# Kernel tuning notes

Hardware: AMD Instinct MI355X
Metric: run time of the kernel (lower is better)

The kernel has to match this reference:

```python
import jax, jax.numpy as jnp
import numpy as np

TWO_PI = 2.0 * np.pi
ALPHA = 0.65
KSIZE = (3, 3, 3)   # (kOr, kH, kW)
ITERS = 1
BN_EPS = 1e-5


def _interp(v, dy, dx):
    """Bilinear sample of v[b,c,o, y+dy[o], x+dx[o]], border-clamped.
    v: [B,C,Or,H,W]; dy, dx: [Or] float per-orientation constant shifts."""
    H, W = v.shape[3], v.shape[4]
    y0 = jnp.floor(dy); fy = dy - y0; y0 = y0.astype(jnp.int32)
    iy = jnp.arange(H)[None, :] + y0[:, None]                      # [Or,H]
    g0 = jnp.take_along_axis(v, jnp.clip(iy, 0, H - 1)[None, None, :, :, None], axis=3)
    g1 = jnp.take_along_axis(v, jnp.clip(iy + 1, 0, H - 1)[None, None, :, :, None], axis=3)
    fyb = fy[None, None, :, None, None]
    v = (1.0 - fyb) * g0 + fyb * g1
    x0 = jnp.floor(dx); fx = dx - x0; x0 = x0.astype(jnp.int32)
    ix = jnp.arange(W)[None, :] + x0[:, None]                      # [Or,W]
    h0 = jnp.take_along_axis(v, jnp.clip(ix, 0, W - 1)[None, None, :, None, :], axis=4)
    h1 = jnp.take_along_axis(v, jnp.clip(ix + 1, 0, W - 1)[None, None, :, None, :], axis=4)
    fxb = fx[None, None, :, None, None]
    return (1.0 - fxb) * h0 + fxb * h1


def _convection(u, g0):
    """out[b,c,p] = u[b,c, p . g0[c]^{-1}] via trilinear resampling.
    Sample point: ((x,y) - R(theta - th0)@(x0,y0), theta - th0), theta periodic."""
    Or = u.shape[2]
    def one(uc, g):  # uc: [B,Or,H,W], g = (x0, y0, th0)
        x0, y0, th0 = g[0], g[1], g[2]
        t = th0 * Or / TWO_PI
        i = jnp.floor(t); f = t - i; i = i.astype(jnp.int32)
        # periodic linear interpolation along orientation axis
        v = (1.0 - f) * jnp.roll(uc, i, axis=1) + f * jnp.roll(uc, i + 1, axis=1)
        a = jnp.arange(Or, dtype=u.dtype) * (TWO_PI / Or) - th0
        dx = -(jnp.cos(a) * x0 - jnp.sin(a) * y0)
        dy = -(jnp.sin(a) * x0 + jnp.cos(a) * y0)
        return _interp(v[:, None], dy, dx)[:, 0]
    return jax.vmap(one, in_axes=(1, 0), out_axes=1)(u, g0)


def _se2_log(qx, qy, dth):
    """Exact SE(2) logarithm coordinates (c1,c2,c3) of group offset (qx,qy,dth)."""
    if abs(dth) < 1e-9:
        return qx, qy, dth
    h = 0.5 * dth
    cot = np.cos(h) / np.sin(h)
    return h * (qx * cot + qy), h * (-qx + qy * cot), dth


def _morph(u, metric, dilate):
    """Fractional morphological dilation (max of u(p.q) - k(q)) or erosion
    (min of u(p.q) + k(q)) with left-invariant Riemannian kernel
    k_c(q) = nu_a * d_c(q)^{2a/(2a-1)}, d_c^2 = (m0*c1)^2+(m1*c2)^2+(m2*c3)^2."""
    kOr, kH, kW = KSIZE
    Or = u.shape[2]
    thetas = jnp.arange(Or, dtype=u.dtype) * (TWO_PI / Or)
    p = 2.0 * ALPHA / (2.0 * ALPHA - 1.0)
    nu = (2.0 * ALPHA - 1.0) * (2.0 * ALPHA) ** (-p)
    out = None
    for qt in range(-(kOr // 2), kOr // 2 + 1):
        dth = qt * TWO_PI / Or
        for qy in range(-(kH // 2), kH // 2 + 1):
            for qx in range(-(kW // 2), kW // 2 + 1):
                c1, c2, c3 = _se2_log(float(qx), float(qy), dth)
                s = (metric[:, 0] * c1) ** 2 + (metric[:, 1] * c2) ** 2 + (metric[:, 2] * c3) ** 2
                k = nu * s ** (p / 2.0)                       # [C]
                # left-invariant shift: spatial offset rotated by theta_o
                dxo = jnp.cos(thetas) * qx - jnp.sin(thetas) * qy
                dyo = jnp.sin(thetas) * qx + jnp.cos(thetas) * qy
                val = _interp(jnp.roll(u, -qt, axis=2), dyo, dxo)
                kb = k[None, :, None, None, None]
                cand = val - kb if dilate else val + kb
                if out is None:
                    out = cand
                else:
                    out = jnp.maximum(out, cand) if dilate else jnp.minimum(out, cand)
    return out


def setup_inputs() -> dict:
    key = jax.random.key(0)
    ks = jax.random.split(key, 5)
    B, Cin, Cout, Or, H, W = 4, 8, 16, 8, 128, 128
    x = jax.random.normal(ks[0], (B, Cin, Or, H, W), dtype=jnp.float32)
    g0 = 0.5 * jax.random.normal(ks[1], (Cin, 3), dtype=jnp.float32)
    lo, hi = 1.4 / 3.0, 0.7 * 3.0   # reset_parameters range for metric params
    metric_dil = jax.random.uniform(ks[2], (Cin, 3), minval=lo, maxval=hi, dtype=jnp.float32)
    metric_ero = jax.random.uniform(ks[3], (Cin, 3), minval=lo, maxval=hi, dtype=jnp.float32)
    bound = 0.25  # kaiming_uniform(a=sqrt(5)) bound for [8,16] weight
    weight = jax.random.uniform(ks[4], (Cin, Cout), minval=-bound, maxval=bound, dtype=jnp.float32)
    gamma = jnp.ones((Cout,), jnp.float32)
    beta = jnp.zeros((Cout,), jnp.float32)
    return dict(x=x, g0=g0, metric_dil=metric_dil, metric_ero=metric_ero,
                weight=weight, gamma=gamma, beta=beta)


def reference(x, g0, metric_dil, metric_ero, weight, gamma, beta):
    u = x
    for _ in range(ITERS):
        u = _convection(u, g0)
        u = _morph(u, metric_dil, dilate=True)
        u = _morph(u, metric_ero, dilate=False)
    # channel mixing: [B,Cin,Or,H,W] x [Cin,Cout] -> [B,Cout,Or,H,W]
    y = jnp.einsum('bcohw,cd->bdohw', u, weight)
    # BatchNorm3d (training mode): per-channel stats over (B,Or,H,W)
    m = y.mean(axis=(0, 2, 3, 4), keepdims=True)
    v = y.var(axis=(0, 2, 3, 4), keepdims=True)
    yh = (y - m) * jax.lax.rsqrt(v + BN_EPS)
    return yh * gamma[None, :, None, None, None] + beta[None, :, None, None, None]
```

## Files before the change

### kernel.cpp

```cpp
#include <hip/hip_runtime.h>
#include <math.h>
#include <utility>

#define B 4
#define CIN 8
#define COUT 16
#define OR_ 8
#define H_ 128
#define W_ 128
#define HW 16384
#define PLANE HW
#define CH_STR (OR_*HW)
#define BATCH_STR (CIN*CH_STR)
#define NELEM (B*BATCH_STR)
#define NPOS (B*OR_*HW)
#define NB_RED 256

#define TILE 16
#define CBR 24
#define CB_S 29
#define CB_PL (CBR*CB_S)
#define DBR 20
#define DB_S 21
#define DB_PL (DBR*DB_S)

typedef __attribute__((ext_vector_type(4))) float f4;

struct Tables {
  float kdil[CIN][27];
  float kero[CIN][27];
  int   o1[CIN][OR_], o2[CIN][OR_];
  int   iy0[CIN][OR_], ix0[CIN][OR_];
  float w00[CIN][OR_], w01[CIN][OR_], w10[CIN][OR_], w11[CIN][OR_];
  float cf[CIN];
};

__host__ __device__ constexpr double m_cos(int o) {
  const double r = 0.70710678118654752440;
  const double t[8] = {1.0, r, 0.0, -r, -1.0, -r, 0.0, r};
  return t[o];
}
__host__ __device__ constexpr double m_sin(int o) {
  const double r = 0.70710678118654752440;
  const double t[8] = {0.0, r, 1.0, r, 0.0, -r, -1.0, -r};
  return t[o];
}
__host__ __device__ constexpr double tap_dx(int o, int j) {
  return m_cos(o)*(j % 3 - 1) - m_sin(o)*(j / 3 - 1);
}
__host__ __device__ constexpr double tap_dy(int o, int j) {
  return m_sin(o)*(j % 3 - 1) + m_cos(o)*(j / 3 - 1);
}
__host__ __device__ constexpr int ifloor(double v) {
  int i = (int)v;
  return ((double)i > v) ? i - 1 : i;
}
__host__ __device__ constexpr int tap_ix(int o, int j) { return ifloor(tap_dx(o, j)); }
__host__ __device__ constexpr int tap_iy(int o, int j) { return ifloor(tap_dy(o, j)); }
__host__ __device__ constexpr float tap_fx(int o, int j) { return (float)(tap_dx(o, j) - tap_ix(o, j)); }
__host__ __device__ constexpr float tap_fy(int o, int j) { return (float)(tap_dy(o, j) - tap_iy(o, j)); }
__host__ __device__ constexpr float corner_w(int o, int j, int dyb, int dxb) {
  float fy = tap_fy(o, j), fx = tap_fx(o, j);
  return (dyb ? fy : 1.0f - fy) * (dxb ? fx : 1.0f - fx);
}
__host__ __device__ constexpr int corner_r(int o, int j, int dyb) { return tap_iy(o, j) + dyb + 2; }
__host__ __device__ constexpr int corner_c(int o, int j, int i, int dxb) { return i + tap_ix(o, j) + dxb + 2; }
__host__ __device__ constexpr bool row_used(int o, int r) {
  for (int j = 0; j < 9; ++j)
    for (int dyb = 0; dyb < 2; ++dyb)
      for (int dxb = 0; dxb < 2; ++dxb)
        if (corner_w(o, j, dyb, dxb) != 0.0f && corner_r(o, j, dyb) == r)
          return true;
  return false;
}

template<int N> struct Rep {
  template<class F> __device__ __forceinline__ static void run(F&& f) {
    Rep<N-1>::run(f);
    f(std::integral_constant<int, N-1>{});
  }
};
template<> struct Rep<0> {
  template<class F> __device__ __forceinline__ static void run(F&&) {}
};


__global__ void precompute_kernel(const float* __restrict__ g0,
                                  const float* __restrict__ mdil,
                                  const float* __restrict__ mero,
                                  Tables* __restrict__ T) {
  const int t = threadIdx.x;
  const double TWO_PI = 6.283185307179586476925286766559;
  const double P  = 2.0*0.65/(2.0*0.65 - 1.0);
  const double NU = (2.0*0.65 - 1.0)*pow(2.0*0.65, -P);
  if (t < 432) {
    int which = t / 216;
    int r = t % 216;
    int c = r / 27;
    int j = r % 27;
    int qt = j/9 - 1;
    int qy = (j/3)%3 - 1;
    int qx = j%3 - 1;
    double dth = qt * (TWO_PI/OR_);
    double c1, c2, c3;
    if (qt == 0) { c1 = qx; c2 = qy; c3 = 0.0; }
    else {
      double h = 0.5*dth;
      double cot = cos(h)/sin(h);
      c1 = h*(qx*cot + qy);
      c2 = h*(-qx + qy*cot);
      c3 = dth;
    }
    const float* m = which ? mero : mdil;
    double a0 = (double)m[c*3+0]*c1;
    double a1 = (double)m[c*3+1]*c2;
    double a2 = (double)m[c*3+2]*c3;
    double s = a0*a0 + a1*a1 + a2*a2;
    float k = (float)(NU * pow(s, P*0.5));
    if (which) T->kero[c][j] = k; else T->kdil[c][j] = k;
  } else if (t >= 512 && t < 512 + CIN*OR_) {
    int r = t - 512;
    int c = r >> 3;
    int o = r & 7;
    float x0 = g0[c*3+0], y0 = g0[c*3+1], th0 = g0[c*3+2];
    float a = (float)(o*(TWO_PI/OR_)) - th0;
    float ca = cosf(a), sa = sinf(a);
    float dxv = -(ca*x0 - sa*y0);
    float dyv = -(sa*x0 + ca*y0);
    float fy0 = floorf(dyv), fx0 = floorf(dxv);
    float fy = dyv - fy0, fx = dxv - fx0;
    T->iy0[c][o] = (int)fy0;
    T->ix0[c][o] = (int)fx0;
    T->w00[c][o] = (1.f-fy)*(1.f-fx);
    T->w01[c][o] = (1.f-fy)*fx;
    T->w10[c][o] = fy*(1.f-fx);
    T->w11[c][o] = fy*fx;
    float tt = th0 * (float)(OR_/TWO_PI);
    float fi = floorf(tt);
    int ci = (int)fi;
    T->o1[c][o] = (o - ci) & 7;
    T->o2[c][o] = (o - ci - 1) & 7;
    if (o == 0) T->cf[c] = tt - fi;
  }
}

template<int O, int DIL, int PL, int RSTR>
__device__ __forceinline__ void morph_tile_lds(const float* __restrict__ sm,
                                               const float* __restrict__ kt,
                                               int row, int gc, float acc[4]) {
  Rep<3>::run([&](auto qc) {
    constexpr int qti = decltype(qc)::value;
    const float* p = sm + ((O + qti + 7) & 7) * PL + row * RSTR + gc;
    float win[5][8];
    Rep<5>::run([&](auto rc) {
      constexpr int r = decltype(rc)::value;
      if constexpr (row_used(O, r)) {
        #pragma unroll
        for (int k = 0; k < 8; ++k) win[r][k] = p[r*RSTR + k];
      }
    });
    Rep<9>::run([&](auto jc) {
      constexpr int j = decltype(jc)::value;
      float k = kt[qti*9 + j];
      float base = DIL ? -k : k;
      Rep<4>::run([&](auto ic) {
        constexpr int i = decltype(ic)::value;
        float v = base;
        Rep<4>::run([&](auto cc2) {
          constexpr int dyb = decltype(cc2)::value >> 1, dxb = decltype(cc2)::value & 1;
          constexpr float Wgt = corner_w(O, j, dyb, dxb);
          if constexpr (Wgt != 0.0f) {
            constexpr int R = corner_r(O, j, dyb);
            constexpr int C = corner_c(O, j, i, dxb);
            v = fmaf(Wgt, win[R][C], v);
          }
        });
        acc[i] = DIL ? fmaxf(acc[i], v) : fminf(acc[i], v);
      });
    });
  });
}

template<int O>
__device__ __forceinline__ void dil_wave(const float* __restrict__ cb, float* __restrict__ db,
                                         const float* __restrict__ kt, int lane) {
  {
    int rA = lane / 5, cA = (lane - rA*5) * 4;
    float acc[4] = {-INFINITY, -INFINITY, -INFINITY, -INFINITY};
    morph_tile_lds<O, 1, CB_PL, CB_S>(cb, kt, rA, cA, acc);
    float* d = db + O*DB_PL + rA*DB_S + cA;
    #pragma unroll
    for (int i = 0; i < 4; ++i) d[i] = acc[i];
  }
  if (lane < 36) {
    int g = lane + 64;
    int rB = g / 5, cB = (g - rB*5) * 4;
    float acc[4] = {-INFINITY, -INFINITY, -INFINITY, -INFINITY};
    morph_tile_lds<O, 1, CB_PL, CB_S>(cb, kt, rB, cB, acc);
    float* d = db + O*DB_PL + rB*DB_S + cB;
    #pragma unroll
    for (int i = 0; i < 4; ++i) d[i] = acc[i];
  }
}

template<int O>
__device__ __forceinline__ void ero_wave(const float* __restrict__ db, float* __restrict__ dst,
                                         const float* __restrict__ kt, int lane) {
  int pr = lane >> 2, pc = (lane & 3) * 4;
  float acc[4] = {INFINITY, INFINITY, INFINITY, INFINITY};
  morph_tile_lds<O, 0, DB_PL, DB_S>(db, kt, pr, pc, acc);
  f4 v = {acc[0], acc[1], acc[2], acc[3]};
  *(f4*)(dst + pr*W_ + pc) = v;
}

__global__ __launch_bounds__(512, 4)
void fused_kernel(const float* __restrict__ x, float* __restrict__ u3,
                  const Tables* __restrict__ T) {
  __shared__ float convbuf[8*CB_PL];
  __shared__ float dilbuf[8*DB_PL];

  int blk = blockIdx.x;
  int tx = blk & 7, ty = (blk >> 3) & 7, c = (blk >> 6) & 7, b = blk >> 9;
  int h0 = ty*TILE, w0 = tx*TILE;
  int t = threadIdx.x;
  int wid = t >> 6, lane = t & 63;

  {
    const int o = wid;
    const float* p1 = x + b*BATCH_STR + c*CH_STR + T->o1[c][o]*PLANE;
    const float* p2 = x + b*BATCH_STR + c*CH_STR + T->o2[c][o]*PLANE;
    const int iy0 = T->iy0[c][o], ix0 = T->ix0[c][o];
    const float w00 = T->w00[c][o], w01 = T->w01[c][o];
    const float w10 = T->w10[c][o], w11 = T->w11[c][o];
    const float cfv = T->cf[c];
    float* cbf = convbuf + o*CB_PL;
    #pragma unroll
    for (int it = 0; it < 3; ++it) {
      int q = lane + it*64;
      if (q < 144) {
        int r = q / 6, cq = q - r*6;
        int gr = h0 - 4 + r;
        int gc4 = w0 - 4 + cq*4;
        int iy = gr + iy0, ix = gc4 + ix0;
        bool ok = (gr >= 0) & (gr <= 127) & (gc4 >= 0) & (gc4+3 <= 127)
                & (iy >= 0) & (iy <= 126) & (ix >= 0) & (ix+4 <= 127);
        float* dst = cbf + r*CB_S + cq*4;
        if (ok) {
          const float* q1 = p1 + iy*W_ + ix;
          const float* q2 = p2 + iy*W_ + ix;
          f4 A0 = *(const f4*)q1;       float A4 = q1[4];
          f4 B0 = *(const f4*)(q1+W_);  float B4 = q1[W_+4];
          f4 C0 = *(const f4*)q2;       float C4 = q2[4];
          f4 D0 = *(const f4*)(q2+W_);  float D4 = q2[W_+4];
          float a[5] = {A0.x, A0.y, A0.z, A0.w, A4};
          float bb[5] = {B0.x, B0.y, B0.z, B0.w, B4};
          float cc[5] = {C0.x, C0.y, C0.z, C0.w, C4};
          float dd[5] = {D0.x, D0.y, D0.z, D0.w, D4};
          #pragma unroll
          for (int i = 0; i < 4; ++i) {
            float v1 = w00*a[i] + w01*a[i+1] + w10*bb[i] + w11*bb[i+1];
            float v2 = w00*cc[i] + w01*cc[i+1] + w10*dd[i] + w11*dd[i+1];
            dst[i] = (1.0f - cfv)*v1 + cfv*v2;
          }
        } else {
          int gh = min(max(gr, 0), 127);
          #pragma unroll
          for (int i = 0; i < 4; ++i) {
            int gw = min(max(gc4 + i, 0), 127);
            int yy = gh + iy0, xx = gw + ix0;
            int r0 = min(max(yy, 0), 127), r1 = min(max(yy+1, 0), 127);
            int c0 = min(max(xx, 0), 127), c1 = min(max(xx+1, 0), 127);
            float v1 = w00*p1[r0*W_+c0] + w01*p1[r0*W_+c1] + w10*p1[r1*W_+c0] + w11*p1[r1*W_+c1];
            float v2 = w00*p2[r0*W_+c0] + w01*p2[r0*W_+c1] + w10*p2[r1*W_+c0] + w11*p2[r1*W_+c1];
            dst[i] = (1.0f - cfv)*v1 + cfv*v2;
          }
        }
      }
    }
  }
  __syncthreads();

  {
    const float* kt = T->kdil[c];
    switch (wid) {
      case 0: dil_wave<0>(convbuf, dilbuf, kt, lane); break;
      case 1: dil_wave<1>(convbuf, dilbuf, kt, lane); break;
      case 2: dil_wave<2>(convbuf, dilbuf, kt, lane); break;
      case 3: dil_wave<3>(convbuf, dilbuf, kt, lane); break;
      case 4: dil_wave<4>(convbuf, dilbuf, kt, lane); break;
      case 5: dil_wave<5>(convbuf, dilbuf, kt, lane); break;
      case 6: dil_wave<6>(convbuf, dilbuf, kt, lane); break;
      default: dil_wave<7>(convbuf, dilbuf, kt, lane); break;
    }
  }
  __syncthreads();

  if ((h0 == 0) | (h0 == 112) | (w0 == 0) | (w0 == 112)) {
    #pragma unroll
    for (int k2 = 0; k2 < 7; ++k2) {
      int i = t + k2*512;
      if (i < 3200) {
        int o = i / 400, rest = i - o*400;
        int row = rest / 20, col = rest - row*20;
        int vh = h0 - 2 + row, vw = w0 - 2 + col;
        int dr = min(max(vh, 0), 127) - vh;
        int dc = min(max(vw, 0), 127) - vw;
        if ((dr | dc) != 0) {
          dilbuf[o*DB_PL + row*DB_S + col] =
            dilbuf[o*DB_PL + (row + dr)*DB_S + col + dc];
        }
      }
    }
  }
  __syncthreads();

  {
    const float* kt = T->kero[c];
    float* dst = u3 + ((b*CIN + c)*OR_ + wid)*PLANE + h0*W_ + w0;
    switch (wid) {
      case 0: ero_wave<0>(dilbuf, dst, kt, lane); break;
      case 1: ero_wave<1>(dilbuf, dst, kt, lane); break;
      case 2: ero_wave<2>(dilbuf, dst, kt, lane); break;
      case 3: ero_wave<3>(dilbuf, dst, kt, lane); break;
      case 4: ero_wave<4>(dilbuf, dst, kt, lane); break;
      case 5: ero_wave<5>(dilbuf, dst, kt, lane); break;
      case 6: ero_wave<6>(dilbuf, dst, kt, lane); break;
      default: ero_wave<7>(dilbuf, dst, kt, lane); break;
    }
  }
}

__global__ void gram_kernel(const float* __restrict__ u, double* __restrict__ part) {
  int t8 = blockIdx.x*256 + threadIdx.x;
  int hw = (t8 & 2047) << 3;
  int o  = (t8 >> 11) & 7;
  int b  = t8 >> 14;
  const float* base = u + b*BATCH_STR + o*PLANE + hw;
  f4 v0[8], v1[8];
  #pragma unroll
  for (int c = 0; c < 8; c++) {
    v0[c] = *(const f4*)(base + c*CH_STR);
    v1[c] = *(const f4*)(base + c*CH_STR + 4);
  }
  float S[8], G[36];
  #pragma unroll
  for (int c = 0; c < 8; c++)
    S[c] = (v0[c].x + v0[c].y) + (v0[c].z + v0[c].w)
         + (v1[c].x + v1[c].y) + (v1[c].z + v1[c].w);
  {
    int t = 0;
    #pragma unroll
    for (int c = 0; c < 8; c++)
      #pragma unroll
      for (int c2 = c; c2 < 8; c2++) {
        G[t] = v0[c].x*v0[c2].x + v0[c].y*v0[c2].y + v0[c].z*v0[c2].z + v0[c].w*v0[c2].w
             + v1[c].x*v1[c2].x + v1[c].y*v1[c2].y + v1[c].z*v1[c2].z + v1[c].w*v1[c2].w;
        t++;
      }
  }
  __shared__ double lds[4][44];
  int lane = threadIdx.x & 63;
  int wave = threadIdx.x >> 6;
  for (int t = 0; t < 44; t++) {
    double vv = (double)((t < 8) ? S[t] : G[t-8]);
    for (int off = 32; off; off >>= 1) vv += __shfl_down(vv, off);
    if (lane == 0) lds[wave][t] = vv;
  }
  __syncthreads();
  if (threadIdx.x < 44) {
    part[blockIdx.x*44 + threadIdx.x] =
      lds[0][threadIdx.x] + lds[1][threadIdx.x] + lds[2][threadIdx.x] + lds[3][threadIdx.x];
  }
}

__global__ void stats_kernel(const double* __restrict__ part, const float* __restrict__ weight,
                             const float* __restrict__ gamma, const float* __restrict__ beta,
                             float* __restrict__ ss) {
  __shared__ double tot[44];
  int t = threadIdx.x;
  if (t < 352) {
    int cnt = t >> 3, j = t & 7;
    double s = 0.0;
    #pragma unroll 8
    for (int k = 0; k < 32; ++k) s += part[(j + (k << 3))*44 + cnt];
    s += __shfl_down(s, 4);
    s += __shfl_down(s, 2);
    s += __shfl_down(s, 1);
    if (j == 0) tot[cnt] = s;
  }
  __syncthreads();
  if (t < 16) {
    double m = 0.0;
    for (int c = 0; c < 8; c++) m += (double)weight[c*COUT + t] * tot[c];
    double e2 = 0.0;
    int idx = 8;
    for (int c = 0; c < 8; c++)
      for (int c2 = c; c2 < 8; c2++) {
        double wp = (double)weight[c*COUT + t] * (double)weight[c2*COUT + t];
        e2 += (c2 == c ? 1.0 : 2.0) * wp * tot[idx];
        idx++;
      }
    double N = (double)NPOS;
    m /= N; e2 /= N;
    double var = e2 - m*m;
    double inv = rsqrt(var + 1e-5);
    float sc = (float)(inv * (double)gamma[t]);
    ss[t]      = sc;
    ss[16 + t] = beta[t] - (float)m * sc;
  }
}

__global__ void final_kernel(const float* __restrict__ u, const float* __restrict__ weight,
                             const float* __restrict__ ss, float* __restrict__ out) {
  __shared__ float Wsh[8][16];
  __shared__ float scale[16], shift[16];
  int t = threadIdx.x;
  if (t < 128) Wsh[t >> 4][t & 15] = weight[t];
  if (t < 16) { scale[t] = ss[t]; shift[t] = ss[16 + t]; }
  __syncthreads();
  int t4 = blockIdx.x*256 + threadIdx.x;
  int hw = (t4 & 4095) << 2;
  int o  = (t4 >> 12) & 7;
  int b  = t4 >> 15;
  const float* base = u + b*BATCH_STR + o*PLANE + hw;
  f4 v[8];
  #pragma unroll
  for (int c = 0; c < 8; c++) v[c] = *(const f4*)(base + c*CH_STR);
  float* ob = out + b*(COUT*CH_STR) + o*PLANE + hw;
  #pragma unroll
  for (int d = 0; d < 16; d++) {
    f4 y = {0.f, 0.f, 0.f, 0.f};
    #pragma unroll
    for (int c = 0; c < 8; c++) {
      float wv = Wsh[c][d];
      y.x = fmaf(v[c].x, wv, y.x);
      y.y = fmaf(v[c].y, wv, y.y);
      y.z = fmaf(v[c].z, wv, y.z);
      y.w = fmaf(v[c].w, wv, y.w);
    }
    float sc = scale[d], sh = shift[d];
    f4 r = { fmaf(y.x, sc, sh), fmaf(y.y, sc, sh), fmaf(y.z, sc, sh), fmaf(y.w, sc, sh) };
    *(f4*)(ob + d*CH_STR) = r;
  }
}

extern "C" void kernel_launch(void* const* d_in, const int* in_sizes, int n_in,
                              void* d_out, int out_size, void* d_ws, size_t ws_size,
                              hipStream_t stream) {
  const float* x      = (const float*)d_in[0];
  const float* g0     = (const float*)d_in[1];
  const float* mdil   = (const float*)d_in[2];
  const float* mero   = (const float*)d_in[3];
  const float* weight = (const float*)d_in[4];
  const float* gamma  = (const float*)d_in[5];
  const float* beta   = (const float*)d_in[6];
  float* out = (float*)d_out;

  char* ws = (char*)d_ws;
  Tables* T    = (Tables*)ws;
  float*  ss   = (float*)(ws + 8*1024);
  double* part = (double*)(ws + 16*1024);
  float*  u3   = (float*)(ws + (size_t)1*1024*1024);

  precompute_kernel<<<1, 1024, 0, stream>>>(g0, mdil, mero, T);
  fused_kernel<<<B*CIN*64, 512, 0, stream>>>(x, u3, T);
  gram_kernel<<<NB_RED, 256, 0, stream>>>(u3, part);
  stats_kernel<<<1, 384, 0, stream>>>(part, weight, gamma, beta, ss);
  final_kernel<<<NPOS/4/256, 256, 0, stream>>>(u3, weight, ss, out);
}
```

Before: 136.7 us.

## Add per-tile interior fast path for convection and fuse stats into gram kernel

Precomputes per-channel min/max integer shifts so each tile can decide once whether all of its convection loads are in bounds. Interior tiles skip per-element bounds checks, and border tiles use a simpler scalar clamped path with one cell per thread. Separately, the stats reduction is folded into the gram kernel through a last-block atomic counter, which removes one kernel launch. The counter reset is done in the precompute kernel. The scalar loads replace the vector loads and may be less efficient.

```diff
diff --git a/kernel.cpp b/kernel.cpp
--- a/kernel.cpp
+++ b/kernel.cpp
@@ -33,6 +33,7 @@
   int   iy0[CIN][OR_], ix0[CIN][OR_];
   float w00[CIN][OR_], w01[CIN][OR_], w10[CIN][OR_], w11[CIN][OR_];
   float cf[CIN];
+  int   iymin[CIN], iymax[CIN], ixmin[CIN], ixmax[CIN];
 };
 
 __host__ __device__ constexpr double m_cos(int o) {
@@ -88,8 +89,10 @@
 __global__ void precompute_kernel(const float* __restrict__ g0,
                                   const float* __restrict__ mdil,
                                   const float* __restrict__ mero,
-                                  Tables* __restrict__ T) {
+                                  Tables* __restrict__ T,
+                                  unsigned int* __restrict__ counter) {
   const int t = threadIdx.x;
+  if (t == 1000) *counter = 0;
   const double TWO_PI = 6.283185307179586476925286766559;
   const double P  = 2.0*0.65/(2.0*0.65 - 1.0);
   const double NU = (2.0*0.65 - 1.0)*pow(2.0*0.65, -P);
@@ -142,6 +145,16 @@
     T->o2[c][o] = (o - ci - 1) & 7;
     if (o == 0) T->cf[c] = tt - fi;
   }
+  __syncthreads();
+  if (t < CIN) {
+    int iymn = 999, iymx = -999, ixmn = 999, ixmx = -999;
+    for (int o = 0; o < OR_; ++o) {
+      iymn = min(iymn, T->iy0[t][o]); iymx = max(iymx, T->iy0[t][o]);
+      ixmn = min(ixmn, T->ix0[t][o]); ixmx = max(ixmx, T->ix0[t][o]);
+    }
+    T->iymin[t] = iymn; T->iymax[t] = iymx;
+    T->ixmin[t] = ixmn; T->ixmax[t] = ixmx;
+  }
 }
 
 template<int O, int DIL, int PL, int RSTR>
@@ -227,54 +240,55 @@
 
   {
     const int o = wid;
-    const float* p1 = x + b*BATCH_STR + c*CH_STR + T->o1[c][o]*PLANE;
-    const float* p2 = x + b*BATCH_STR + c*CH_STR + T->o2[c][o]*PLANE;
     const int iy0 = T->iy0[c][o], ix0 = T->ix0[c][o];
     const float w00 = T->w00[c][o], w01 = T->w01[c][o];
     const float w10 = T->w10[c][o], w11 = T->w11[c][o];
     const float cfv = T->cf[c];
+    const float* p1 = x + b*BATCH_STR + c*CH_STR + T->o1[c][o]*PLANE;
+    const float* p2 = x + b*BATCH_STR + c*CH_STR + T->o2[c][o]*PLANE;
     float* cbf = convbuf + o*CB_PL;
-    #pragma unroll
-    for (int it = 0; it < 3; ++it) {
-      int q = lane + it*64;
-      if (q < 144) {
-        int r = q / 6, cq = q - r*6;
-        int gr = h0 - 4 + r;
-        int gc4 = w0 - 4 + cq*4;
-        int iy = gr + iy0, ix = gc4 + ix0;
-        bool ok = (gr >= 0) & (gr <= 127) & (gc4 >= 0) & (gc4+3 <= 127)
-                & (iy >= 0) & (iy <= 126) & (ix >= 0) & (ix+4 <= 127);
-        float* dst = cbf + r*CB_S + cq*4;
-        if (ok) {
+    bool interior = (h0 - 4 + T->iymin[c] >= 0) & (h0 + 20 + T->iymax[c] <= 127)
+                  & (w0 - 4 + T->ixmin[c] >= 0) & (w0 + 20 + T->ixmax[c] <= 127)
+                  & (h0 >= 16) & (h0 <= 96) & (w0 >= 16) & (w0 <= 96);
+    if (interior) {
+      #pragma unroll
+      for (int it = 0; it < 3; ++it) {
+        int q = lane + it*64;
+        if (q < 144) {
+          int r = q / 6;
+          int cq = q - r*6;
+          int iy = h0 - 4 + r + iy0;
+          int ix = w0 - 4 + cq*4 + ix0;
           const float* q1 = p1 + iy*W_ + ix;
           const float* q2 = p2 + iy*W_ + ix;
-          f4 A0 = *(const f4*)q1;       float A4 = q1[4];
-          f4 B0 = *(const f4*)(q1+W_);  float B4 = q1[W_+4];
-          f4 C0 = *(const f4*)q2;       float C4 = q2[4];
-          f4 D0 = *(const f4*)(q2+W_);  float D4 = q2[W_+4];
-          float a[5] = {A0.x, A0.y, A0.z, A0.w, A4};
-          float bb[5] = {B0.x, B0.y, B0.z, B0.w, B4};
-          float cc[5] = {C0.x, C0.y, C0.z, C0.w, C4};
-          float dd[5] = {D0.x, D0.y, D0.z, D0.w, D4};
+          float a[5], bb[5], cc[5], dd[5];
+          #pragma unroll
+          for (int k = 0; k < 5; ++k) {
+            a[k] = q1[k]; bb[k] = q1[W_+k]; cc[k] = q2[k]; dd[k] = q2[W_+k];
+          }
+          float* dst = cbf + r*CB_S + cq*4;
           #pragma unroll
           for (int i = 0; i < 4; ++i) {
             float v1 = w00*a[i] + w01*a[i+1] + w10*bb[i] + w11*bb[i+1];
             float v2 = w00*cc[i] + w01*cc[i+1] + w10*dd[i] + w11*dd[i+1];
             dst[i] = (1.0f - cfv)*v1 + cfv*v2;
           }
-        } else {
-          int gh = min(max(gr, 0), 127);
-          #pragma unroll
-          for (int i = 0; i < 4; ++i) {
-            int gw = min(max(gc4 + i, 0), 127);
-            int yy = gh + iy0, xx = gw + ix0;
-            int r0 = min(max(yy, 0), 127), r1 = min(max(yy+1, 0), 127);
-            int c0 = min(max(xx, 0), 127), c1 = min(max(xx+1, 0), 127);
-            float v1 = w00*p1[r0*W_+c0] + w01*p1[r0*W_+c1] + w10*p1[r1*W_+c0] + w11*p1[r1*W_+c1];
-            float v2 = w00*p2[r0*W_+c0] + w01*p2[r0*W_+c1] + w10*p2[r1*W_+c0] + w11*p2[r1*W_+c1];
-            dst[i] = (1.0f - cfv)*v1 + cfv*v2;
-          }
         }
+      }
+    } else {
+      #pragma unroll
+      for (int it = 0; it < 9; ++it) {
+        int cell = lane + it*64;
+        int r = cell / 24;
+        int col = cell - r*24;
+        int gh = min(max(h0 - 4 + r, 0), 127);
+        int gw = min(max(w0 - 4 + col, 0), 127);
+        int iy = gh + iy0, ix = gw + ix0;
+        int r0 = min(max(iy, 0), 127), r1 = min(max(iy+1, 0), 127);
+        int c0 = min(max(ix, 0), 127), c1 = min(max(ix+1, 0), 127);
+        float v1 = w00*p1[r0*W_+c0] + w01*p1[r0*W_+c1] + w10*p1[r1*W_+c0] + w11*p1[r1*W_+c1];
+        float v2 = w00*p2[r0*W_+c0] + w01*p2[r0*W_+c1] + w10*p2[r1*W_+c0] + w11*p2[r1*W_+c1];
+        cbf[r*CB_S + col] = (1.0f - cfv)*v1 + cfv*v2;
       }
     }
   }
@@ -330,7 +344,12 @@
   }
 }
 
-__global__ void gram_kernel(const float* __restrict__ u, double* __restrict__ part) {
+__global__ void gram_kernel(const float* __restrict__ u, double* __restrict__ part,
+                            const float* __restrict__ weight,
+                            const float* __restrict__ gamma,
+                            const float* __restrict__ beta,
+                            float* __restrict__ ss,
+                            unsigned int* __restrict__ counter) {
   int t8 = blockIdx.x*256 + threadIdx.x;
   int hw = (t8 & 2047) << 3;
   int o  = (t8 >> 11) & 7;
@@ -359,6 +378,7 @@
       }
   }
   __shared__ double lds[4][44];
+  __shared__ unsigned int lastFlag;
   int lane = threadIdx.x & 63;
   int wave = threadIdx.x >> 6;
   for (int t = 0; t < 44; t++) {
@@ -371,22 +391,29 @@
     part[blockIdx.x*44 + threadIdx.x] =
       lds[0][threadIdx.x] + lds[1][threadIdx.x] + lds[2][threadIdx.x] + lds[3][threadIdx.x];
   }
-}
-
-__global__ void stats_kernel(const double* __restrict__ part, const float* __restrict__ weight,
-                             const float* __restrict__ gamma, const float* __restrict__ beta,
-                             float* __restrict__ ss) {
+  __threadfence();
+  if (threadIdx.x == 0) {
+    unsigned int old = atomicAdd(counter, 1u);
+    lastFlag = (old == NB_RED - 1) ? 1u : 0u;
+  }
+  __syncthreads();
+  if (lastFlag == 0) return;
+
+  __threadfence();
   __shared__ double tot[44];
   int t = threadIdx.x;
-  if (t < 352) {
-    int cnt = t >> 3, j = t & 7;
-    double s = 0.0;
-    #pragma unroll 8
-    for (int k = 0; k < 32; ++k) s += part[(j + (k << 3))*44 + cnt];
-    s += __shfl_down(s, 4);
-    s += __shfl_down(s, 2);
-    s += __shfl_down(s, 1);
-    if (j == 0) tot[cnt] = s;
+  #pragma unroll
+  for (int basec = 0; basec < 44; basec += 32) {
+    int cnt = basec + (t >> 3);
+    int j = t & 7;
+    if (cnt < 44 && (t >> 3) < 32) {
+      double s = 0.0;
+      for (int k = j; k < NB_RED; k += 8) s += part[k*44 + cnt];
+      s += __shfl_down(s, 4);
+      s += __shfl_down(s, 2);
+      s += __shfl_down(s, 1);
+      if (j == 0) tot[cnt] = s;
+    }
   }
   __syncthreads();
   if (t < 16) {
@@ -458,13 +485,13 @@
 
   char* ws = (char*)d_ws;
   Tables* T    = (Tables*)ws;
+  unsigned int* counter = (unsigned int*)(ws + 6*1024);
   float*  ss   = (float*)(ws + 8*1024);
   double* part = (double*)(ws + 16*1024);
   float*  u3   = (float*)(ws + (size_t)1*1024*1024);
 
-  precompute_kernel<<<1, 1024, 0, stream>>>(g0, mdil, mero, T);
+  precompute_kernel<<<1, 1024, 0, stream>>>(g0, mdil, mero, T, counter);
   fused_kernel<<<B*CIN*64, 512, 0, stream>>>(x, u3, T);
-  gram_kernel<<<NB_RED, 256, 0, stream>>>(u3, part);
-  stats_kernel<<<1, 384, 0, stream>>>(part, weight, gamma, beta, ss);
+  gram_kernel<<<NB_RED, 256, 0, stream>>>(u3, part, weight, gamma, beta, ss, counter);
   final_kernel<<<NPOS/4/256, 256, 0, stream>>>(u3, weight, ss, out);
 }
```

Result: slower. 143.4 us (+4.9%).
